# Optimization experiments

Hardware: AMD Instinct MI355X
Metric: run time of the kernel (lower is better)

Reference implementation:

```python
import jax, jax.numpy as jnp
import numpy as np

EPS = 1e-5
NEG_SLOPE = 0.2  # GATConv default negative_slope


def layer_norm(x, g, b):
    mu = jnp.mean(x, axis=-1, keepdims=True)
    var = jnp.mean((x - mu) ** 2, axis=-1, keepdims=True)
    return (x - mu) * jax.lax.rsqrt(var + EPS) * g + b


def setup_inputs() -> dict:
    key = jax.random.key(0)
    ks = jax.random.split(key, 16)
    B, NPG = 64, 1024          # graphs, fine nodes per graph
    NF = B * NPG               # 65536 fine nodes
    IN, HID, ATT, H, LLM = 1024, 1024, 64, 8, 2048
    D = ATT * H                # 512
    w = lambda k, shp: (jax.random.normal(k, shp, jnp.float32) * 0.02)
    # structured bipartite star edges: fine node i -> global node i // NPG
    edge_index = jnp.stack([jnp.arange(NF, dtype=jnp.int32),
                            (jnp.arange(NF, dtype=jnp.int32) // NPG)])
    return {
        "x_fine": jax.random.normal(ks[0], (NF, IN), jnp.float32),
        "x_global": jax.random.normal(ks[1], (B, D), jnp.float32),
        "edge_index_fine_global": edge_index,
        "nf_g": jnp.ones((IN,), jnp.float32), "nf_b": jnp.zeros((IN,), jnp.float32),
        "ip_w1": w(ks[2], (IN, HID)), "ip_b1": jnp.zeros((HID,), jnp.float32),
        "ip_w2": w(ks[3], (HID, D)), "ip_b2": jnp.zeros((D,), jnp.float32),
        "ng_g": jnp.ones((D,), jnp.float32), "ng_b": jnp.zeros((D,), jnp.float32),
        "gat_ws": w(ks[4], (D, D)), "gat_wd": w(ks[5], (D, D)),
        "att_s": w(ks[6], (1, H, ATT)), "att_d": w(ks[7], (1, H, ATT)),
        "gat_bias": jnp.zeros((D,), jnp.float32),
        "gp_w": w(ks[8], (D, LLM)), "gp_b": jnp.zeros((LLM,), jnp.float32),
        "fp_w": w(ks[9], (D, LLM)), "fp_b": jnp.zeros((LLM,), jnp.float32),
    }


def reference(x_fine, x_global, edge_index_fine_global,
              nf_g, nf_b, ip_w1, ip_b1, ip_w2, ip_b2, ng_g, ng_b,
              gat_ws, gat_wd, att_s, att_d, gat_bias,
              gp_w, gp_b, fp_w, fp_b):
    B = x_global.shape[0]
    H = att_s.shape[1]
    C = x_global.shape[1] // H

    # fine branch: LayerNorm -> MLP projection to H*C
    xf = layer_norm(x_fine, nf_g, nf_b)
    xf = jax.nn.relu(xf @ ip_w1 + ip_b1) @ ip_w2 + ip_b2      # [NF, H*C]
    xg = layer_norm(x_global, ng_g, ng_b)                      # [B, H*C]

    # bipartite GATConv (eval mode: attention dropout disabled)
    xs = (xf @ gat_ws).reshape(-1, H, C)                       # [NF, H, C]
    xd = (xg @ gat_wd).reshape(B, H, C)                        # [B, H, C]
    a_s = jnp.sum(xs * att_s, axis=-1)                         # [NF, H]
    a_d = jnp.sum(xd * att_d, axis=-1)                         # [B, H]

    row, col = edge_index_fine_global[0], edge_index_fine_global[1]
    loops = jnp.arange(B, dtype=row.dtype)                     # add_self_loops: nodes < min(NF,B)
    rows = jnp.concatenate([row, loops])
    cols = jnp.concatenate([col, loops])
    # PyG removes pre-existing self-loop edges; emulate by masking them out
    self_mask = jnp.concatenate([row == col, jnp.zeros((B,), bool)])

    logits = jax.nn.leaky_relu(a_s[rows] + a_d[cols], NEG_SLOPE)   # [E+B, H]
    logits = jnp.where(self_mask[:, None], -jnp.inf, logits)
    m = jax.ops.segment_max(logits, cols, num_segments=B)         # [B, H]
    e = jnp.exp(logits - m[cols])
    e = jnp.where(self_mask[:, None], 0.0, e)
    denom = jax.ops.segment_sum(e, cols, num_segments=B)
    alpha = e / denom[cols]                                       # [E+B, H]

    msg = xs[rows] * alpha[..., None]                              # [E+B, H, C]
    agg = jax.ops.segment_sum(msg, cols, num_segments=B)          # [B, H, C]
    xg = agg.reshape(B, H * C) + gat_bias + xg                    # GAT out + residual

    og = (xg @ gp_w + gp_b)[:, None, :]                            # [B, 1, LLM]
    of = (xf @ fp_w + fp_b).reshape(B, -1, fp_w.shape[1])          # [B, NPG, LLM]
    return jnp.concatenate([og, of], axis=1)                       # [B, 1+NPG, LLM]
```

## Files before the change

### kernel.cpp

```cpp
#include <hip/hip_runtime.h>
#include <hip/hip_bf16.h>
#include <math.h>

typedef __bf16 bf16_t;
typedef bf16_t bf16x8 __attribute__((ext_vector_type(8)));
typedef bf16_t bf16x4 __attribute__((ext_vector_type(4)));
typedef float f32x4 __attribute__((ext_vector_type(4)));

#define DEVINL __device__ __forceinline__

DEVINL float wave_reduce_sum(float v) {
#pragma unroll
  for (int o = 32; o > 0; o >>= 1) v += __shfl_down(v, o);
  return v;
}
DEVINL float block_reduce_sum256(float v, float* red) {
  int tid = threadIdx.x;
  __syncthreads();
  v = wave_reduce_sum(v);
  if ((tid & 63) == 0) red[tid >> 6] = v;
  __syncthreads();
  return red[0] + red[1] + red[2] + red[3];
}

__global__ __launch_bounds__(256) void k_ln_fine(const float* __restrict__ x,
                                                 const float* __restrict__ g,
                                                 const float* __restrict__ b,
                                                 bf16_t* __restrict__ out) {
  constexpr int CPT = 4, COLS = 1024;
  __shared__ float red[8];
  const size_t row = blockIdx.x;
  const float* xr = x + row * COLS;
  const int c0 = threadIdx.x * CPT;
  float v[CPT];
#pragma unroll
  for (int j = 0; j < CPT; j++) v[j] = xr[c0 + j];
  float s = 0;
#pragma unroll
  for (int j = 0; j < CPT; j++) s += v[j];
  const float mu = block_reduce_sum256(s, red) * (1.0f / COLS);
  float q = 0;
#pragma unroll
  for (int j = 0; j < CPT; j++) { float d = v[j] - mu; q += d * d; }
  const float var = block_reduce_sum256(q, red) * (1.0f / COLS);
  const float rs = rsqrtf(var + 1e-5f);
  bf16x4 o;
#pragma unroll
  for (int j = 0; j < CPT; j++)
    o[j] = (bf16_t)((v[j] - mu) * rs * g[c0 + j] + b[c0 + j]);
  *(bf16x4*)(out + row * COLS + c0) = o;
}

__global__ __launch_bounds__(256) void k_prep(
    const float* __restrict__ ip_w1, const float* __restrict__ ip_w2,
    const float* __restrict__ fp_w, const float* __restrict__ gat_wd,
    const float* __restrict__ att_d, const float* __restrict__ gat_ws,
    const float* __restrict__ att_s, const float* __restrict__ x_global,
    const float* __restrict__ ng_g, const float* __restrict__ ng_b,
    bf16_t* __restrict__ w1t, bf16_t* __restrict__ w2t, bf16_t* __restrict__ fpt,
    float* __restrict__ wd_att, float* __restrict__ wsatt, float* __restrict__ xg) {
  __shared__ float t[32][33];
  __shared__ float red[8];
  const int bid = blockIdx.x, tid = threadIdx.x;
  if (bid < 2560) {
    const float* src;
    bf16_t* dst;
    int N, n0, k0;
    if (bid < 1024) {
      src = ip_w1; dst = w1t; N = 1024;
      n0 = (bid & 31) * 32; k0 = (bid >> 5) * 32;
    } else if (bid < 1536) {
      const int rel = bid - 1024;
      src = ip_w2; dst = w2t; N = 512;
      n0 = (rel & 15) * 32; k0 = (rel >> 4) * 32;
    } else {
      const int rel = bid - 1536;
      src = fp_w; dst = fpt; N = 2048;
      n0 = (rel & 63) * 32; k0 = (rel >> 6) * 32;
    }
    const int K = (bid < 1536) ? 1024 : 512;
    const int tx = tid & 31, ty = tid >> 5;
#pragma unroll
    for (int i = 0; i < 32; i += 8)
      t[ty + i][tx] = src[(size_t)(k0 + ty + i) * N + n0 + tx];
    __syncthreads();
#pragma unroll
    for (int i = 0; i < 32; i += 8)
      dst[(size_t)(n0 + ty + i) * K + k0 + tx] = (bf16_t)t[tx][ty + i];
  } else if (bid < 2564) {
    const int rel = bid - 2560;
    const float* W = (rel < 2) ? gat_wd : gat_ws;
    const float* att = (rel < 2) ? att_d : att_s;
    float* outp = (rel < 2) ? wd_att : wsatt;
    const int k = (rel & 1) * 256 + tid;
#pragma unroll
    for (int h = 0; h < 8; h++) {
      float s = 0;
      for (int c = 0; c < 64; c++)
        s += W[(size_t)k * 512 + h * 64 + c] * att[h * 64 + c];
      outp[k * 8 + h] = s;
    }
  } else {
    const int row = bid - 2564;
    const float* xr = x_global + (size_t)row * 512;
    const int c0 = tid * 2;
    float v0 = xr[c0], v1 = xr[c0 + 1];
    const float mu = block_reduce_sum256(v0 + v1, red) * (1.0f / 512);
    const float d0 = v0 - mu, d1 = v1 - mu;
    const float var = block_reduce_sum256(d0 * d0 + d1 * d1, red) * (1.0f / 512);
    const float rs = rsqrtf(var + 1e-5f);
    xg[(size_t)row * 512 + c0] = d0 * rs * ng_g[c0] + ng_b[c0];
    xg[(size_t)row * 512 + c0 + 1] = d1 * rs * ng_g[c0 + 1] + ng_b[c0 + 1];
  }
}

template <int N, int K, int EPI>
__global__ __launch_bounds__(256, 2) void gemm_bt(const bf16_t* __restrict__ A,
                                                  const bf16_t* __restrict__ Bt,
                                                  const float* __restrict__ bias,
                                                  void* __restrict__ Cout) {
  __shared__ bf16_t As[128 * 64];
  __shared__ bf16_t Bs[128 * 64];
  const int tid = threadIdx.x;
  const int lane = tid & 63;
  const int wid = tid >> 6;
  const int wm = wid >> 1, wn = wid & 1;
  const size_t arow0 = (size_t)blockIdx.x * 128;
  const int bcol0 = blockIdx.y * 128;

  f32x4 acc[4][4] = {};
  const int kTiles = K / 64;
  for (int kt = 0; kt < kTiles; ++kt) {
    const int k0 = kt * 64;
#pragma unroll
    for (int i = 0; i < 4; ++i) {
      const int c = i * 256 + tid;
      const int r = c >> 3, kc = (c & 7) * 8;
      const bf16_t* ga = A + (arow0 + r) * K + k0 + kc;
      __builtin_amdgcn_global_load_lds(
          (const __attribute__((address_space(1))) void*)ga,
          (__attribute__((address_space(3))) void*)(As + c * 8), 16, 0, 0);
      const bf16_t* gb = Bt + ((size_t)bcol0 + r) * K + k0 + kc;
      __builtin_amdgcn_global_load_lds(
          (const __attribute__((address_space(1))) void*)gb,
          (__attribute__((address_space(3))) void*)(Bs + c * 8), 16, 0, 0);
    }
    __syncthreads();
#pragma unroll
    for (int kk = 0; kk < 2; ++kk) {
      bf16x8 af[4], bfr[4];
      const int kofs = kk * 32 + (lane >> 4) * 8;
#pragma unroll
      for (int m = 0; m < 4; ++m)
        af[m] = *(const bf16x8*)(As + (wm * 64 + m * 16 + (lane & 15)) * 64 + kofs);
#pragma unroll
      for (int n = 0; n < 4; ++n)
        bfr[n] = *(const bf16x8*)(Bs + (wn * 64 + n * 16 + (lane & 15)) * 64 + kofs);
#pragma unroll
      for (int m = 0; m < 4; ++m)
#pragma unroll
        for (int n = 0; n < 4; ++n)
          acc[m][n] = __builtin_amdgcn_mfma_f32_16x16x32_bf16(af[m], bfr[n], acc[m][n], 0, 0, 0);
    }
    __syncthreads();
  }
  const int lr = (lane >> 4) * 4;
  const int lc = lane & 15;
#pragma unroll
  for (int n = 0; n < 4; ++n) {
    const int col = bcol0 + wn * 64 + n * 16 + lc;
    const float bv = bias[col];
#pragma unroll
    for (int m = 0; m < 4; ++m) {
#pragma unroll
      for (int j = 0; j < 4; ++j) {
        const size_t row = arow0 + wm * 64 + m * 16 + lr + j;
        float v = acc[m][n][j] + bv;
        if constexpr (EPI == 0) v = v > 0.0f ? v : 0.0f;
        if constexpr (EPI == 3) {
          const size_t orow = row + (row >> 10) + 1;
          ((float*)Cout)[orow * (size_t)N + col] = v;
        } else {
          ((bf16_t*)Cout)[row * (size_t)N + col] = (bf16_t)v;
        }
      }
    }
  }
}

__global__ __launch_bounds__(256) void k_as(const bf16_t* __restrict__ xf,
                                            const float* __restrict__ wsatt,
                                            float* __restrict__ a_s) {
  const int tid = threadIdx.x, l = tid & 63, wid = tid >> 6;
  float wreg[64];
#pragma unroll
  for (int q = 0; q < 16; q++) {
    const float4 v = *(const float4*)(wsatt + l * 64 + q * 4);
    wreg[q * 4 + 0] = v.x; wreg[q * 4 + 1] = v.y;
    wreg[q * 4 + 2] = v.z; wreg[q * 4 + 3] = v.w;
  }
  const size_t base = (size_t)blockIdx.x * 128 + wid * 32;
  for (int rr = 0; rr < 32; rr++) {
    const size_t i = base + rr;
    const bf16x8 v = *(const bf16x8*)(xf + i * 512 + l * 8);
    float p[8] = {};
#pragma unroll
    for (int u = 0; u < 8; u++) {
      const float xv = (float)v[u];
#pragma unroll
      for (int h = 0; h < 8; h++) p[h] += xv * wreg[u * 8 + h];
    }
#pragma unroll
    for (int h = 0; h < 8; h++)
#pragma unroll
      for (int mk = 1; mk < 64; mk <<= 1) p[h] += __shfl_xor(p[h], mk);
    float outv = 0.0f;
#pragma unroll
    for (int h = 0; h < 8; h++) outv = (l == h) ? p[h] : outv;
    if (l < 8) a_s[i * 8 + l] = outv;
  }
}

__global__ __launch_bounds__(512) void k_alpha_z(const float* __restrict__ a_s,
                                                 const bf16_t* __restrict__ xf,
                                                 const float* __restrict__ xg,
                                                 const float* __restrict__ wd_att,
                                                 float* __restrict__ zq) {
  __shared__ float sal[8][260];
  const int b = blockIdx.x >> 2, qq = blockIdx.x & 3;
  const int tid = threadIdx.x, l = tid & 63, h = tid >> 6;
  float pa = 0;
#pragma unroll
  for (int u = 0; u < 8; u++)
    pa += xg[b * 512 + l * 8 + u] * wd_att[(l * 8 + u) * 8 + h];
#pragma unroll
  for (int mk = 1; mk < 64; mk <<= 1) pa += __shfl_xor(pa, mk);
  const float ad = pa;
  const float* asb = a_s + (size_t)b * 1024 * 8;
  float lg[16];
  float lmax = -1e30f;
#pragma unroll
  for (int j = 0; j < 16; j++) {
    const float a = asb[(l + j * 64) * 8 + h] + ad;
    lg[j] = a > 0.0f ? a : 0.2f * a;
    lmax = fmaxf(lmax, lg[j]);
  }
  float lself = -INFINITY;
  if (l == 0 && b != 0) {
    const float a = a_s[b * 8 + h] + ad;
    lself = a > 0.0f ? a : 0.2f * a;
  }
  lmax = fmaxf(lmax, lself);
#pragma unroll
  for (int mk = 1; mk < 64; mk <<= 1) lmax = fmaxf(lmax, __shfl_xor(lmax, mk));
  float ps = 0;
#pragma unroll
  for (int j = 0; j < 16; j++) { lg[j] = __expf(lg[j] - lmax); ps += lg[j]; }
  const float eself = (l == 0 && lself != -INFINITY) ? __expf(lself - lmax) : 0.0f;
  ps += eself;
#pragma unroll
  for (int mk = 1; mk < 64; mk <<= 1) ps += __shfl_xor(ps, mk);
  const float inv = 1.0f / ps;
#pragma unroll
  for (int j = 0; j < 4; j++) sal[h][l + j * 64] = lg[qq * 4 + j] * inv;
  if (l == 0) sal[h][256] = (qq == 0) ? eself * inv : 0.0f;
  __syncthreads();
  float zp[8] = {};
  const bf16_t* xb = xf + ((size_t)b * 1024 + qq * 256) * 512 + l * 8;
  for (int i = 0; i < 256; i += 2) {
    const float a0 = sal[h][i], a1 = sal[h][i + 1];
    const bf16x8 v0 = *(const bf16x8*)(xb + (size_t)i * 512);
    const bf16x8 v1 = *(const bf16x8*)(xb + (size_t)(i + 1) * 512);
#pragma unroll
    for (int u = 0; u < 8; u++) zp[u] += a0 * (float)v0[u] + a1 * (float)v1[u];
  }
  if (qq == 0) {
    const float a = sal[h][256];
    const bf16x8 v = *(const bf16x8*)(xf + (size_t)b * 512 + l * 8);
#pragma unroll
    for (int u = 0; u < 8; u++) zp[u] += a * (float)v[u];
  }
  float4 o0 = {zp[0], zp[1], zp[2], zp[3]};
  float4 o1 = {zp[4], zp[5], zp[6], zp[7]};
  float* zo = zq + (((size_t)b * 4 + qq) * 8 + h) * 512 + l * 8;
  *(float4*)zo = o0;
  *(float4*)(zo + 4) = o1;
}

__global__ __launch_bounds__(512) void k_fin(const float* __restrict__ zq,
                                             const float* __restrict__ ws,
                                             const float* __restrict__ gat_bias,
                                             const float* __restrict__ xg,
                                             float* __restrict__ aggx) {
  __shared__ float zsum[4096];
  const int b = blockIdx.x, c = threadIdx.x, h = c >> 6;
  const float* zb = zq + (size_t)b * 4 * 4096;
  for (int idx = c; idx < 4096; idx += 512)
    zsum[idx] = zb[idx] + zb[4096 + idx] + zb[8192 + idx] + zb[12288 + idx];
  __syncthreads();
  const float* zr = zsum + h * 512;
  float acc = 0;
#pragma unroll 8
  for (int k = 0; k < 512; k++) acc += zr[k] * ws[(size_t)k * 512 + c];
  aggx[b * 512 + c] = acc + gat_bias[c] + xg[b * 512 + c];
}

__global__ __launch_bounds__(256) void k_og(const float* __restrict__ aggx,
                                            const float* __restrict__ gp_w,
                                            const float* __restrict__ gp_b,
                                            float* __restrict__ out) {
  __shared__ float xv[512];
  const int b = blockIdx.y;
  const int c = blockIdx.x * 256 + threadIdx.x;
  for (int k = threadIdx.x; k < 512; k += 256) xv[k] = aggx[b * 512 + k];
  __syncthreads();
  float acc = gp_b[c];
#pragma unroll 8
  for (int k = 0; k < 512; k++) acc += xv[k] * gp_w[(size_t)k * 2048 + c];
  out[(size_t)b * 1025 * 2048 + c] = acc;
}

extern "C" void kernel_launch(void* const* d_in, const int* in_sizes, int n_in,
                              void* d_out, int out_size, void* d_ws, size_t ws_size,
                              hipStream_t stream) {
  const float* x_fine   = (const float*)d_in[0];
  const float* x_global = (const float*)d_in[1];
  const float* nf_g  = (const float*)d_in[3];
  const float* nf_b  = (const float*)d_in[4];
  const float* ip_w1 = (const float*)d_in[5];
  const float* ip_b1 = (const float*)d_in[6];
  const float* ip_w2 = (const float*)d_in[7];
  const float* ip_b2 = (const float*)d_in[8];
  const float* ng_g  = (const float*)d_in[9];
  const float* ng_b  = (const float*)d_in[10];
  const float* gat_ws   = (const float*)d_in[11];
  const float* gat_wd   = (const float*)d_in[12];
  const float* att_s    = (const float*)d_in[13];
  const float* att_d    = (const float*)d_in[14];
  const float* gat_bias = (const float*)d_in[15];
  const float* gp_w = (const float*)d_in[16];
  const float* gp_b = (const float*)d_in[17];
  const float* fp_w = (const float*)d_in[18];
  const float* fp_b = (const float*)d_in[19];
  float* out = (float*)d_out;

  char* ws = (char*)d_ws;
  bf16_t* xf_ln = (bf16_t*)ws;
  bf16_t* hbuf  = (bf16_t*)(ws + 134217728ULL);
  char* sm = ws + 268435456ULL;
  bf16_t* w1t  = (bf16_t*)sm;
  bf16_t* w2t  = (bf16_t*)(sm + 2097152ULL);
  bf16_t* fpt  = (bf16_t*)(sm + 3145728ULL);
  float*  a_s  = (float*)(sm + 5242880ULL);
  float*  xg   = (float*)(sm + 7340032ULL);
  float*  wd_att = (float*)(sm + 7471104ULL);
  float*  wsatt  = (float*)(sm + 7487488ULL);
  float*  zbuf4  = (float*)(sm + 7503872ULL);
  float*  aggx   = (float*)(sm + 11698176ULL);
  bf16_t* xf = xf_ln;

  k_prep<<<2628, 256, 0, stream>>>(ip_w1, ip_w2, fp_w, gat_wd, att_d, gat_ws,
                                   att_s, x_global, ng_g, ng_b, w1t, w2t, fpt,
                                   wd_att, wsatt, xg);

  k_ln_fine<<<65536, 256, 0, stream>>>(x_fine, nf_g, nf_b, xf_ln);

  gemm_bt<1024, 1024, 0><<<dim3(512, 8), 256, 0, stream>>>(xf_ln, w1t, ip_b1, hbuf);
  gemm_bt<512, 1024, 1><<<dim3(512, 4), 256, 0, stream>>>(hbuf, w2t, ip_b2, xf);

  k_as<<<512, 256, 0, stream>>>(xf, wsatt, a_s);
  k_alpha_z<<<256, 512, 0, stream>>>(a_s, xf, xg, wd_att, zbuf4);
  k_fin<<<64, 512, 0, stream>>>(zbuf4, gat_ws, gat_bias, xg, aggx);
  k_og<<<dim3(8, 64), 256, 0, stream>>>(aggx, gp_w, gp_b, out);

  gemm_bt<2048, 512, 3><<<dim3(512, 16), 256, 0, stream>>>(xf, fpt, fp_b, out);
}
```

Baseline: 812.1 us.

## Switch GEMM to 32x32x16 MFMA tiles and fuse GAT finish with global projection

New measurement: 1.005 ms. 1.24x slower.

```diff
diff --git a/kernel.cpp b/kernel.cpp
--- a/kernel.cpp
+++ b/kernel.cpp
@@ -6,6 +6,7 @@
 typedef bf16_t bf16x8 __attribute__((ext_vector_type(8)));
 typedef bf16_t bf16x4 __attribute__((ext_vector_type(4)));
 typedef float f32x4 __attribute__((ext_vector_type(4)));
+typedef float f32x16 __attribute__((ext_vector_type(16)));
 
 #define DEVINL __device__ __forceinline__
 
@@ -127,8 +128,9 @@
   const int wm = wid >> 1, wn = wid & 1;
   const size_t arow0 = (size_t)blockIdx.x * 128;
   const int bcol0 = blockIdx.y * 128;
-
-  f32x4 acc[4][4] = {};
+  const int l31 = lane & 31, hk = lane >> 5;
+
+  f32x16 acc[2][2] = {};
   const int kTiles = K / 64;
   for (int kt = 0; kt < kTiles; ++kt) {
     const int k0 = kt * 64;
@@ -147,35 +149,34 @@
     }
     __syncthreads();
 #pragma unroll
-    for (int kk = 0; kk < 2; ++kk) {
-      bf16x8 af[4], bfr[4];
-      const int kofs = kk * 32 + (lane >> 4) * 8;
-#pragma unroll
-      for (int m = 0; m < 4; ++m)
-        af[m] = *(const bf16x8*)(As + (wm * 64 + m * 16 + (lane & 15)) * 64 + kofs);
-#pragma unroll
-      for (int n = 0; n < 4; ++n)
-        bfr[n] = *(const bf16x8*)(Bs + (wn * 64 + n * 16 + (lane & 15)) * 64 + kofs);
-#pragma unroll
-      for (int m = 0; m < 4; ++m)
-#pragma unroll
-        for (int n = 0; n < 4; ++n)
-          acc[m][n] = __builtin_amdgcn_mfma_f32_16x16x32_bf16(af[m], bfr[n], acc[m][n], 0, 0, 0);
+    for (int kk = 0; kk < 4; ++kk) {
+      bf16x8 af[2], bfr[2];
+      const int ko = kk * 16 + hk * 8;
+#pragma unroll
+      for (int m = 0; m < 2; ++m)
+        af[m] = *(const bf16x8*)(As + (wm * 64 + m * 32 + l31) * 64 + ko);
+#pragma unroll
+      for (int n = 0; n < 2; ++n)
+        bfr[n] = *(const bf16x8*)(Bs + (wn * 64 + n * 32 + l31) * 64 + ko);
+#pragma unroll
+      for (int m = 0; m < 2; ++m)
+#pragma unroll
+        for (int n = 0; n < 2; ++n)
+          acc[m][n] = __builtin_amdgcn_mfma_f32_32x32x16_bf16(af[m], bfr[n], acc[m][n], 0, 0, 0);
     }
     __syncthreads();
   }
-  const int lr = (lane >> 4) * 4;
-  const int lc = lane & 15;
-#pragma unroll
-  for (int n = 0; n < 4; ++n) {
-    const int col = bcol0 + wn * 64 + n * 16 + lc;
+#pragma unroll
+  for (int n = 0; n < 2; ++n) {
+    const int col = bcol0 + wn * 64 + n * 32 + l31;
     const float bv = bias[col];
 #pragma unroll
-    for (int m = 0; m < 4; ++m) {
-#pragma unroll
-      for (int j = 0; j < 4; ++j) {
-        const size_t row = arow0 + wm * 64 + m * 16 + lr + j;
-        float v = acc[m][n][j] + bv;
+    for (int m = 0; m < 2; ++m) {
+#pragma unroll
+      for (int reg = 0; reg < 16; ++reg) {
+        const size_t row =
+            arow0 + wm * 64 + m * 32 + (reg & 3) + 8 * (reg >> 2) + 4 * hk;
+        float v = acc[m][n][reg] + bv;
         if constexpr (EPI == 0) v = v > 0.0f ? v : 0.0f;
         if constexpr (EPI == 3) {
           const size_t orow = row + (row >> 10) + 1;
@@ -287,12 +288,15 @@
   *(float4*)(zo + 4) = o1;
 }
 
-__global__ __launch_bounds__(512) void k_fin(const float* __restrict__ zq,
-                                             const float* __restrict__ ws,
-                                             const float* __restrict__ gat_bias,
-                                             const float* __restrict__ xg,
-                                             float* __restrict__ aggx) {
+__global__ __launch_bounds__(512) void k_finog(const float* __restrict__ zq,
+                                               const float* __restrict__ ws,
+                                               const float* __restrict__ gat_bias,
+                                               const float* __restrict__ xg,
+                                               const float* __restrict__ gp_w,
+                                               const float* __restrict__ gp_b,
+                                               float* __restrict__ out) {
   __shared__ float zsum[4096];
+  __shared__ float aggx[512];
   const int b = blockIdx.x, c = threadIdx.x, h = c >> 6;
   const float* zb = zq + (size_t)b * 4 * 4096;
   for (int idx = c; idx < 4096; idx += 512)
@@ -302,22 +306,16 @@
   float acc = 0;
 #pragma unroll 8
   for (int k = 0; k < 512; k++) acc += zr[k] * ws[(size_t)k * 512 + c];
-  aggx[b * 512 + c] = acc + gat_bias[c] + xg[b * 512 + c];
-}
-
-__global__ __launch_bounds__(256) void k_og(const float* __restrict__ aggx,
-                                            const float* __restrict__ gp_w,
-                                            const float* __restrict__ gp_b,
-                                            float* __restrict__ out) {
-  __shared__ float xv[512];
-  const int b = blockIdx.y;
-  const int c = blockIdx.x * 256 + threadIdx.x;
-  for (int k = threadIdx.x; k < 512; k += 256) xv[k] = aggx[b * 512 + k];
-  __syncthreads();
-  float acc = gp_b[c];
+  aggx[c] = acc + gat_bias[c] + xg[b * 512 + c];
+  __syncthreads();
+#pragma unroll
+  for (int j = 0; j < 4; j++) {
+    const int cc = c + j * 512;
+    float o = gp_b[cc];
 #pragma unroll 8
-  for (int k = 0; k < 512; k++) acc += xv[k] * gp_w[(size_t)k * 2048 + c];
-  out[(size_t)b * 1025 * 2048 + c] = acc;
+    for (int k = 0; k < 512; k++) o += aggx[k] * gp_w[(size_t)k * 2048 + cc];
+    out[(size_t)b * 1025 * 2048 + cc] = o;
+  }
 }
 
 extern "C" void kernel_launch(void* const* d_in, const int* in_sizes, int n_in,
@@ -356,7 +354,6 @@
   float*  wd_att = (float*)(sm + 7471104ULL);
   float*  wsatt  = (float*)(sm + 7487488ULL);
   float*  zbuf4  = (float*)(sm + 7503872ULL);
-  float*  aggx   = (float*)(sm + 11698176ULL);
   bf16_t* xf = xf_ln;
 
   k_prep<<<2628, 256, 0, stream>>>(ip_w1, ip_w2, fp_w, gat_wd, att_d, gat_ws,
@@ -370,8 +367,7 @@
 
   k_as<<<512, 256, 0, stream>>>(xf, wsatt, a_s);
   k_alpha_z<<<256, 512, 0, stream>>>(a_s, xf, xg, wd_att, zbuf4);
-  k_fin<<<64, 512, 0, stream>>>(zbuf4, gat_ws, gat_bias, xg, aggx);
-  k_og<<<dim3(8, 64), 256, 0, stream>>>(aggx, gp_w, gp_b, out);
+  k_finog<<<64, 512, 0, stream>>>(zbuf4, gat_ws, gat_bias, xg, gp_w, gp_b, out);
 
   gemm_bt<2048, 512, 3><<<dim3(512, 16), 256, 0, stream>>>(xf, fpt, fp_b, out);
 }
```
